# Performance work log

Measured on AMD Instinct MI355X. Metric: run time of the kernel, lower is better.

Reference implementation:

```python
import jax, jax.numpy as jnp
import numpy as np


def setup_inputs() -> dict:
    key = jax.random.key(0)
    k1, k2, k3 = jax.random.split(key, 3)
    B, D, R, O = 8192, 2048, 16, 64
    # small init scale so the 2048-step matrix chain product stays numerically sane
    inputs = jax.random.normal(k1, (B, D), dtype=jnp.float32) * 0.05
    # cores near identity (glorot-scale perturbation) to avoid chain blow-up/collapse
    cores = jnp.eye(R, dtype=jnp.float32)[None] + jax.random.normal(k2, (D, R, R), dtype=jnp.float32) * (1.0 / R)
    projection = jax.random.normal(k3, (R, O), dtype=jnp.float32) * (1.0 / np.sqrt(R))
    bias = jnp.zeros((O,), dtype=jnp.float32)
    return {"inputs": inputs, "cores": cores, "projection": projection, "bias": bias}


def reference(inputs, cores, projection, bias):
    # inputs: (B, D); cores: (D, R, R); projection: (R, O); bias: (O,)
    B = inputs.shape[0]
    R = cores.shape[-1]
    boundary0 = jnp.ones((B, R), dtype=inputs.dtype)  # MPS boundary vector

    x_t = inputs.T  # (D, B) so scan iterates over features

    def step(boundary, xs):
        core, x = xs  # core: (R, R), x: (B,)
        # boundary <- (boundary @ core) scaled by the feature value (A^i[x_i])
        boundary = jnp.matmul(boundary, core) * x[:, None]
        return boundary, None

    boundary, _ = jax.lax.scan(step, boundary0, (cores, x_t))
    out = jnp.matmul(boundary, projection) + bias  # (B, O)
    return out
```

## Files before the change

kernel.cpp:

```cpp
#include <hip/hip_runtime.h>
#include <math.h>


#define DFEAT 2048
#define R 16
#define NR2 256
#define OUTD 64
#define CHUNK 64
#define NCHUNK (DFEAT / CHUNK)
#define MAGIC 0x7E57C0DE

__device__ __forceinline__ float4 rowmul(const float* Arow, const float* B,
                                         int c0) {
    float4 acc = {0.f, 0.f, 0.f, 0.f};
    const float4* a4 = (const float4*)Arow;
#pragma unroll
    for (int kk = 0; kk < 4; ++kk) {
        const float4 av = a4[kk];
        const float4 b0 = *(const float4*)&B[(4 * kk + 0) * 16 + c0];
        const float4 b1 = *(const float4*)&B[(4 * kk + 1) * 16 + c0];
        const float4 b2 = *(const float4*)&B[(4 * kk + 2) * 16 + c0];
        const float4 b3 = *(const float4*)&B[(4 * kk + 3) * 16 + c0];
        acc.x = fmaf(av.x, b0.x, fmaf(av.y, b1.x, fmaf(av.z, b2.x, fmaf(av.w, b3.x, acc.x))));
        acc.y = fmaf(av.x, b0.y, fmaf(av.y, b1.y, fmaf(av.z, b2.y, fmaf(av.w, b3.y, acc.y))));
        acc.z = fmaf(av.x, b0.z, fmaf(av.y, b1.z, fmaf(av.z, b2.z, fmaf(av.w, b3.z, acc.z))));
        acc.w = fmaf(av.x, b0.w, fmaf(av.y, b1.w, fmaf(av.z, b2.w, fmaf(av.w, b3.w, acc.w))));
    }
    return acc;
}

__global__ __launch_bounds__(256) void mps_fused(const float* __restrict__ cores,
                                                 const float* __restrict__ proj,
                                                 const float* __restrict__ x,
                                                 float* __restrict__ prodbuf,
                                                 float* __restrict__ partials,
                                                 int* __restrict__ flags,
                                                 float* __restrict__ pE,
                                                 int B) {
    __shared__ __align__(16) float S[4608];
    float* Bbase = S;
    float* Abase = S + 2048;
    float* Fbase = S + 4096;
    float* Pt    = S;

    const int tid  = threadIdx.x;
    const int wave = tid >> 6, lane = tid & 63;

    if (blockIdx.x >= NCHUNK) {
        const int row = (blockIdx.x - NCHUNK) * 4 + wave;
        if (row >= B) return;
        const float4* xr = (const float4*)(x + (size_t)row * DFEAT);
        float prod = 1.f;
#pragma unroll
        for (int it = 0; it < DFEAT / (64 * 4); ++it) {
            float4 v = xr[it * 64 + lane];
            prod *= (v.x * v.y) * (v.z * v.w);
        }
#pragma unroll
        for (int off = 32; off > 0; off >>= 1)
            prod *= __shfl_xor(prod, off);
        if (lane == 0) prodbuf[row] = prod;
        return;
    }

    const int ri = lane >> 2;
    const int c0 = (lane & 3) << 2;
    const size_t d0 = (size_t)blockIdx.x * CHUNK;

    const float* gw = cores + (d0 + 16 * wave) * NR2;
    float4 pre[16];
#pragma unroll
    for (int t = 0; t < 16; ++t)
        pre[t] = *(const float4*)&gw[(size_t)t * NR2 + lane * 4];

    float* AwW = Abase + wave * 512;
    float* BbW = Bbase + wave * 512;

    *(float4*)&AwW[0 * 256 + lane * 4] = pre[0];
    int cur = 0;
#pragma unroll
    for (int t = 1; t < 16; ++t) {
        *(float4*)&BbW[(t & 1) * 256 + lane * 4] = pre[t];
        float4 r = rowmul(&AwW[cur * 256 + ri * 16], &BbW[(t & 1) * 256], c0);
        *(float4*)&AwW[(cur ^ 1) * 256 + ri * 16 + c0] = r;
        cur ^= 1;
    }
    __syncthreads();

    if (wave == 0) {
        *(float4*)&Fbase[0 * 256 + ri * 16 + c0] =
            *(const float4*)&Abase[0 * 512 + 1 * 256 + ri * 16 + c0];
        int cc = 0;
        for (int w = 1; w < 4; ++w) {
            float4 r = rowmul(&Fbase[cc * 256 + ri * 16],
                              &Abase[w * 512 + 1 * 256], c0);
            *(float4*)&Fbase[(cc ^ 1) * 256 + ri * 16 + c0] = r;
            cc ^= 1;
        }
    }
    __syncthreads();
    const int i = tid >> 4, j = tid & 15;
    const float v = Fbase[1 * 256 + tid];

    if (blockIdx.x != 0) {
        partials[blockIdx.x * NR2 + tid] = v;
        __syncthreads();
        if (tid == 0)
            __hip_atomic_store(&flags[blockIdx.x], MAGIC,
                               __ATOMIC_RELEASE, __HIP_MEMORY_SCOPE_AGENT);
        return;
    }

    Pt[0 * 256 + j * 16 + i] = v;

    {
        const int f = 1 + (tid % (NCHUNK - 1));
        while (__hip_atomic_load(&flags[f], __ATOMIC_ACQUIRE,
                                 __HIP_MEMORY_SCOPE_AGENT) != MAGIC) { }
    }
    __syncthreads();

    float w = 1.f;
    int E = 0;
    for (int rr = 0; rr < 4; ++rr) {
#pragma unroll
        for (int q = 0; q < 2; ++q) {
            const int idx = q * 256 + tid;
            const int flat = idx * 4;
            const int s = flat >> 8;
            if (rr > 0 || s > 0) {
                float4 p4 =
                    ((const float4*)(partials + (size_t)(8 * rr) * NR2))[idx];
                const int e = flat & 255;
                const int k = e >> 4, j0 = e & 15;
                Pt[s * 256 + (j0 + 0) * 16 + k] = p4.x;
                Pt[s * 256 + (j0 + 1) * 16 + k] = p4.y;
                Pt[s * 256 + (j0 + 2) * 16 + k] = p4.z;
                Pt[s * 256 + (j0 + 3) * 16 + k] = p4.w;
            }
        }
        __syncthreads();
        if (tid < 64) {
            const int jj = tid & 15, q = tid >> 4;
            for (int s = 0; s < 8; ++s) {
                const float4 pr = *(const float4*)&Pt[s * 256 + jj * 16 + 4 * q];
                float sum;
                sum = __shfl(w, 4 * q + 0) * pr.x;
                sum = fmaf(__shfl(w, 4 * q + 1), pr.y, sum);
                sum = fmaf(__shfl(w, 4 * q + 2), pr.z, sum);
                sum = fmaf(__shfl(w, 4 * q + 3), pr.w, sum);
                sum += __shfl_xor(sum, 16);
                sum += __shfl_xor(sum, 32);
                w = sum;
            }
            float m = fabsf(w);
#pragma unroll
            for (int off = 1; off <= 8; off <<= 1)
                m = fmaxf(m, __shfl_xor(m, off));
            if (m > 0.f) {
                int e2 = 0;
                (void)frexpf(m, &e2);
                w = ldexpf(w, -e2);
                E += e2;
            }
        }
        __syncthreads();
    }

    if (tid < 64) {
        float p = 0.f;
#pragma unroll
        for (int k = 0; k < R; ++k)
            p = fmaf(__shfl(w, k), proj[k * OUTD + tid], p);
        pE[tid] = p;
        if (tid == 0) ((int*)pE)[OUTD] = E;
    }
}

__global__ __launch_bounds__(256) void mps_scale(const float* __restrict__ prodbuf,
                                                 const float* __restrict__ pE,
                                                 const float* __restrict__ bias,
                                                 float* __restrict__ out,
                                                 int B) {
    const int idx = blockIdx.x * 256 + threadIdx.x;
    const int total4 = B * (OUTD / 4);
    if (idx >= total4) return;
    const int row = idx >> 4;
    const int c4  = idx & 15;
    const float pr = prodbuf[row];
    const int   E  = ((const int*)pE)[OUTD];
    const float4 pe = ((const float4*)pE)[c4];
    const float4 bb = ((const float4*)bias)[c4];
    float4 r;
    r.x = ldexpf(pe.x * pr, E) + bb.x;
    r.y = ldexpf(pe.y * pr, E) + bb.y;
    r.z = ldexpf(pe.z * pr, E) + bb.z;
    r.w = ldexpf(pe.w * pr, E) + bb.w;
    ((float4*)out)[idx] = r;
}

extern "C" void kernel_launch(void* const* d_in, const int* in_sizes, int n_in,
                              void* d_out, int out_size, void* d_ws, size_t ws_size,
                              hipStream_t stream) {
    const float* inputs = (const float*)d_in[0];
    const float* cores  = (const float*)d_in[1];
    const float* proj   = (const float*)d_in[2];
    const float* bias   = (const float*)d_in[3];
    float* out = (float*)d_out;

    const int B = in_sizes[0] / DFEAT;

    float* prodbuf  = (float*)d_ws;
    float* partials = prodbuf + B;
    float* pE    = partials + NCHUNK * NR2;
    int*   flags = (int*)(pE + 68);

    const int rowBlocks = (B + 3) / 4;
    mps_fused<<<NCHUNK + rowBlocks, 256, 0, stream>>>(cores, proj, inputs,
                                                      prodbuf, partials, flags,
                                                      pE, B);
    mps_scale<<<(B * 16 + 255) / 256, 256, 0, stream>>>(prodbuf, pE, bias,
                                                        out, B);
}
```

Measured before the change: 103.7 us.

## Fuse output scaling into main kernel using per-unit readiness flags

Merges the separate scaling kernel into the main kernel: row-product blocks publish per-unit flags, and each of the 32 chain blocks waits for its rows and for the final projected vector, then writes its slice of the output. This removes a kernel launch and the inter-kernel gap. In exchange, output writing is confined to 32 blocks, and spin-waits and stale-flag reliance across calls add risk.

```diff
diff --git a/kernel.cpp b/kernel.cpp
--- a/kernel.cpp
+++ b/kernel.cpp
@@ -29,14 +29,17 @@
     return acc;
 }
 
-__global__ __launch_bounds__(256) void mps_fused(const float* __restrict__ cores,
-                                                 const float* __restrict__ proj,
-                                                 const float* __restrict__ x,
-                                                 float* __restrict__ prodbuf,
-                                                 float* __restrict__ partials,
-                                                 int* __restrict__ flags,
-                                                 float* __restrict__ pE,
-                                                 int B) {
+__global__ __launch_bounds__(256, 8) void mps_one(const float* __restrict__ cores,
+                                                  const float* __restrict__ proj,
+                                                  const float* __restrict__ x,
+                                                  const float* __restrict__ bias,
+                                                  float* __restrict__ out,
+                                                  float* __restrict__ prodbuf,
+                                                  float* __restrict__ partials,
+                                                  int* __restrict__ flags,
+                                                  int* __restrict__ uflags,
+                                                  float* __restrict__ pE,
+                                                  int B) {
     __shared__ __align__(16) float S[4608];
     float* Bbase = S;
     float* Abase = S + 2048;
@@ -45,10 +48,13 @@
 
     const int tid  = threadIdx.x;
     const int wave = tid >> 6, lane = tid & 63;
-
-    if (blockIdx.x >= NCHUNK) {
-        const int row = (blockIdx.x - NCHUNK) * 4 + wave;
-        if (row >= B) return;
+    const int bid  = blockIdx.x;
+    const int nunits = B >> 2;
+    const int UPC = nunits / NCHUNK;
+
+    if (bid >= NCHUNK) {
+        const int u = bid - NCHUNK;
+        const int row = u * 4 + wave;
         const float4* xr = (const float4*)(x + (size_t)row * DFEAT);
         float prod = 1.f;
 #pragma unroll
@@ -60,12 +66,16 @@
         for (int off = 32; off > 0; off >>= 1)
             prod *= __shfl_xor(prod, off);
         if (lane == 0) prodbuf[row] = prod;
+        __syncthreads();
+        if (tid == 0)
+            __hip_atomic_store(&uflags[u], MAGIC,
+                               __ATOMIC_RELEASE, __HIP_MEMORY_SCOPE_AGENT);
         return;
     }
 
     const int ri = lane >> 2;
     const int c0 = (lane & 3) << 2;
-    const size_t d0 = (size_t)blockIdx.x * CHUNK;
+    const size_t d0 = (size_t)bid * CHUNK;
 
     const float* gw = cores + (d0 + 16 * wave) * NR2;
     float4 pre[16];
@@ -102,101 +112,122 @@
     const int i = tid >> 4, j = tid & 15;
     const float v = Fbase[1 * 256 + tid];
 
-    if (blockIdx.x != 0) {
-        partials[blockIdx.x * NR2 + tid] = v;
+    if (bid != 0) {
+        partials[bid * NR2 + tid] = v;
         __syncthreads();
         if (tid == 0)
-            __hip_atomic_store(&flags[blockIdx.x], MAGIC,
+            __hip_atomic_store(&flags[bid], MAGIC,
                                __ATOMIC_RELEASE, __HIP_MEMORY_SCOPE_AGENT);
-        return;
-    }
-
-    Pt[0 * 256 + j * 16 + i] = v;
-
-    {
-        const int f = 1 + (tid % (NCHUNK - 1));
-        while (__hip_atomic_load(&flags[f], __ATOMIC_ACQUIRE,
-                                 __HIP_MEMORY_SCOPE_AGENT) != MAGIC) { }
-    }
-    __syncthreads();
-
-    float w = 1.f;
-    int E = 0;
-    for (int rr = 0; rr < 4; ++rr) {
-#pragma unroll
-        for (int q = 0; q < 2; ++q) {
-            const int idx = q * 256 + tid;
-            const int flat = idx * 4;
-            const int s = flat >> 8;
-            if (rr > 0 || s > 0) {
-                float4 p4 =
-                    ((const float4*)(partials + (size_t)(8 * rr) * NR2))[idx];
-                const int e = flat & 255;
-                const int k = e >> 4, j0 = e & 15;
-                Pt[s * 256 + (j0 + 0) * 16 + k] = p4.x;
-                Pt[s * 256 + (j0 + 1) * 16 + k] = p4.y;
-                Pt[s * 256 + (j0 + 2) * 16 + k] = p4.z;
-                Pt[s * 256 + (j0 + 3) * 16 + k] = p4.w;
+    } else {
+        Pt[0 * 256 + j * 16 + i] = v;
+
+        {
+            const int f = 1 + (tid % (NCHUNK - 1));
+            while (__hip_atomic_load(&flags[f], __ATOMIC_ACQUIRE,
+                                     __HIP_MEMORY_SCOPE_AGENT) != MAGIC) { }
+        }
+        __syncthreads();
+
+        float w = 1.f;
+        int E = 0;
+        for (int rr = 0; rr < 4; ++rr) {
+#pragma unroll
+            for (int q = 0; q < 2; ++q) {
+                const int idx = q * 256 + tid;
+                const int flat = idx * 4;
+                const int s = flat >> 8;
+                if (rr > 0 || s > 0) {
+                    float4 p4 = ((const float4*)(partials +
+                                   (size_t)(8 * rr) * NR2))[idx];
+                    const int e = flat & 255;
+                    const int k = e >> 4, j0 = e & 15;
+                    Pt[s * 256 + (j0 + 0) * 16 + k] = p4.x;
+                    Pt[s * 256 + (j0 + 1) * 16 + k] = p4.y;
+                    Pt[s * 256 + (j0 + 2) * 16 + k] = p4.z;
+                    Pt[s * 256 + (j0 + 3) * 16 + k] = p4.w;
+                }
             }
-        }
-        __syncthreads();
+            __syncthreads();
+            if (tid < 64) {
+                const int jj = tid & 15, q = tid >> 4;
+                for (int s = 0; s < 8; ++s) {
+                    const float4 pr =
+                        *(const float4*)&Pt[s * 256 + jj * 16 + 4 * q];
+                    float sum;
+                    sum = __shfl(w, 4 * q + 0) * pr.x;
+                    sum = fmaf(__shfl(w, 4 * q + 1), pr.y, sum);
+                    sum = fmaf(__shfl(w, 4 * q + 2), pr.z, sum);
+                    sum = fmaf(__shfl(w, 4 * q + 3), pr.w, sum);
+                    sum += __shfl_xor(sum, 16);
+                    sum += __shfl_xor(sum, 32);
+                    w = sum;
+                }
+                float m = fabsf(w);
+#pragma unroll
+                for (int off = 1; off <= 8; off <<= 1)
+                    m = fmaxf(m, __shfl_xor(m, off));
+                if (m > 0.f) {
+                    int e2 = 0;
+                    (void)frexpf(m, &e2);
+                    w = ldexpf(w, -e2);
+                    E += e2;
+                }
+            }
+            __syncthreads();
+        }
+
         if (tid < 64) {
-            const int jj = tid & 15, q = tid >> 4;
-            for (int s = 0; s < 8; ++s) {
-                const float4 pr = *(const float4*)&Pt[s * 256 + jj * 16 + 4 * q];
-                float sum;
-                sum = __shfl(w, 4 * q + 0) * pr.x;
-                sum = fmaf(__shfl(w, 4 * q + 1), pr.y, sum);
-                sum = fmaf(__shfl(w, 4 * q + 2), pr.z, sum);
-                sum = fmaf(__shfl(w, 4 * q + 3), pr.w, sum);
-                sum += __shfl_xor(sum, 16);
-                sum += __shfl_xor(sum, 32);
-                w = sum;
-            }
-            float m = fabsf(w);
-#pragma unroll
-            for (int off = 1; off <= 8; off <<= 1)
-                m = fmaxf(m, __shfl_xor(m, off));
-            if (m > 0.f) {
-                int e2 = 0;
-                (void)frexpf(m, &e2);
-                w = ldexpf(w, -e2);
-                E += e2;
-            }
-        }
-        __syncthreads();
+            float p = 0.f;
+#pragma unroll
+            for (int k = 0; k < R; ++k)
+                p = fmaf(__shfl(w, k), proj[k * OUTD + tid], p);
+            pE[tid] = p;
+            if (tid == 0) ((int*)pE)[OUTD] = E;
+        }
+        __syncthreads();
+        if (tid == 0)
+            __hip_atomic_store(&flags[0], MAGIC,
+                               __ATOMIC_RELEASE, __HIP_MEMORY_SCOPE_AGENT);
     }
 
     if (tid < 64) {
-        float p = 0.f;
-#pragma unroll
-        for (int k = 0; k < R; ++k)
-            p = fmaf(__shfl(w, k), proj[k * OUTD + tid], p);
-        pE[tid] = p;
-        if (tid == 0) ((int*)pE)[OUTD] = E;
-    }
-}
-
-__global__ __launch_bounds__(256) void mps_scale(const float* __restrict__ prodbuf,
-                                                 const float* __restrict__ pE,
-                                                 const float* __restrict__ bias,
-                                                 float* __restrict__ out,
-                                                 int B) {
-    const int idx = blockIdx.x * 256 + threadIdx.x;
-    const int total4 = B * (OUTD / 4);
-    if (idx >= total4) return;
-    const int row = idx >> 4;
-    const int c4  = idx & 15;
-    const float pr = prodbuf[row];
-    const int   E  = ((const int*)pE)[OUTD];
-    const float4 pe = ((const float4*)pE)[c4];
-    const float4 bb = ((const float4*)bias)[c4];
-    float4 r;
-    r.x = ldexpf(pe.x * pr, E) + bb.x;
-    r.y = ldexpf(pe.y * pr, E) + bb.y;
-    r.z = ldexpf(pe.z * pr, E) + bb.z;
-    r.w = ldexpf(pe.w * pr, E) + bb.w;
-    ((float4*)out)[idx] = r;
+        for (int i2 = tid; i2 < UPC; i2 += 64) {
+            while (__hip_atomic_load(&uflags[bid * UPC + i2], __ATOMIC_ACQUIRE,
+                                     __HIP_MEMORY_SCOPE_AGENT) != MAGIC)
+                __builtin_amdgcn_s_sleep(16);
+        }
+    } else if (tid == 64) {
+        while (__hip_atomic_load(&flags[0], __ATOMIC_ACQUIRE,
+                                 __HIP_MEMORY_SCOPE_AGENT) != MAGIC)
+            __builtin_amdgcn_s_sleep(16);
+    }
+    __syncthreads();
+    (void)__hip_atomic_load(&flags[0], __ATOMIC_ACQUIRE,
+                            __HIP_MEMORY_SCOPE_AGENT);
+
+    if (tid < 16) {
+        ((float4*)&Fbase[0])[tid]  = ((const float4*)pE)[tid];
+        ((float4*)&Fbase[64])[tid] = ((const float4*)bias)[tid];
+    }
+    if (tid == 16) ((int*)&Fbase[128])[0] = ((const int*)pE)[OUTD];
+    __syncthreads();
+    const int   E  = ((const int*)&Fbase[128])[0];
+    const float4 pe = ((const float4*)&Fbase[0])[tid & 15];
+    const float4 bb = ((const float4*)&Fbase[64])[tid & 15];
+
+    const int chunk4 = B * (OUTD / 4) / NCHUNK;
+    const int base4  = bid * chunk4;
+    float4* o4 = (float4*)out;
+    for (int q = 0; q < chunk4 / 256; ++q) {
+        const int idx = base4 + q * 256 + tid;
+        const float pr = prodbuf[idx >> 4];
+        float4 r;
+        r.x = ldexpf(pe.x * pr, E) + bb.x;
+        r.y = ldexpf(pe.y * pr, E) + bb.y;
+        r.z = ldexpf(pe.z * pr, E) + bb.z;
+        r.w = ldexpf(pe.w * pr, E) + bb.w;
+        o4[idx] = r;
+    }
 }
 
 extern "C" void kernel_launch(void* const* d_in, const int* in_sizes, int n_in,
@@ -214,11 +245,10 @@
     float* partials = prodbuf + B;
     float* pE    = partials + NCHUNK * NR2;
     int*   flags = (int*)(pE + 68);
-
-    const int rowBlocks = (B + 3) / 4;
-    mps_fused<<<NCHUNK + rowBlocks, 256, 0, stream>>>(cores, proj, inputs,
-                                                      prodbuf, partials, flags,
-                                                      pE, B);
-    mps_scale<<<(B * 16 + 255) / 256, 256, 0, stream>>>(prodbuf, pE, bias,
-                                                        out, B);
+    int*   uflags = flags + NCHUNK;
+
+    const int nunits = B / 4;
+    mps_one<<<NCHUNK + nunits, 256, 0, stream>>>(cores, proj, inputs, bias,
+                                                 out, prodbuf, partials,
+                                                 flags, uflags, pE, B);
 }
```

Result: slower. 164.5 us (+58.6%).

## Split chain kernel from row products and fuse row product with output scaling

Applied to the files above, without the earlier changes.

The row-product blocks move out of the chain-reduction kernel into a new per-row kernel. That kernel computes each row's product of x and writes the scaled, biased output directly. This removes the prodbuf intermediate and its write/read round trip. The trade-off is that the bandwidth-heavy read of x no longer overlaps with the latency-bound chain reduction; it now runs serially after it.

```diff
diff --git a/kernel.cpp b/kernel.cpp
--- a/kernel.cpp
+++ b/kernel.cpp
@@ -29,14 +29,11 @@
     return acc;
 }
 
-__global__ __launch_bounds__(256) void mps_fused(const float* __restrict__ cores,
+__global__ __launch_bounds__(256) void mps_chain(const float* __restrict__ cores,
                                                  const float* __restrict__ proj,
-                                                 const float* __restrict__ x,
-                                                 float* __restrict__ prodbuf,
                                                  float* __restrict__ partials,
                                                  int* __restrict__ flags,
-                                                 float* __restrict__ pE,
-                                                 int B) {
+                                                 float* __restrict__ pE) {
     __shared__ __align__(16) float S[4608];
     float* Bbase = S;
     float* Abase = S + 2048;
@@ -45,24 +42,6 @@
 
     const int tid  = threadIdx.x;
     const int wave = tid >> 6, lane = tid & 63;
-
-    if (blockIdx.x >= NCHUNK) {
-        const int row = (blockIdx.x - NCHUNK) * 4 + wave;
-        if (row >= B) return;
-        const float4* xr = (const float4*)(x + (size_t)row * DFEAT);
-        float prod = 1.f;
-#pragma unroll
-        for (int it = 0; it < DFEAT / (64 * 4); ++it) {
-            float4 v = xr[it * 64 + lane];
-            prod *= (v.x * v.y) * (v.z * v.w);
-        }
-#pragma unroll
-        for (int off = 32; off > 0; off >>= 1)
-            prod *= __shfl_xor(prod, off);
-        if (lane == 0) prodbuf[row] = prod;
-        return;
-    }
-
     const int ri = lane >> 2;
     const int c0 = (lane & 3) << 2;
     const size_t d0 = (size_t)blockIdx.x * CHUNK;
@@ -177,26 +156,30 @@
     }
 }
 
-__global__ __launch_bounds__(256) void mps_scale(const float* __restrict__ prodbuf,
-                                                 const float* __restrict__ pE,
-                                                 const float* __restrict__ bias,
-                                                 float* __restrict__ out,
-                                                 int B) {
-    const int idx = blockIdx.x * 256 + threadIdx.x;
-    const int total4 = B * (OUTD / 4);
-    if (idx >= total4) return;
-    const int row = idx >> 4;
-    const int c4  = idx & 15;
-    const float pr = prodbuf[row];
+__global__ __launch_bounds__(256) void mps_rows(const float* __restrict__ x,
+                                                const float* __restrict__ pE,
+                                                const float* __restrict__ bias,
+                                                float* __restrict__ out,
+                                                int B) {
+    const int gtid = blockIdx.x * 256 + threadIdx.x;
+    const int row  = gtid >> 6;
+    const int lane = threadIdx.x & 63;
+    if (row >= B) return;
+
+    const float4* xr = (const float4*)(x + (size_t)row * DFEAT);
+    float prod = 1.f;
+#pragma unroll
+    for (int it = 0; it < DFEAT / (64 * 4); ++it) {
+        float4 v = xr[it * 64 + lane];
+        prod *= (v.x * v.y) * (v.z * v.w);
+    }
+#pragma unroll
+    for (int off = 32; off > 0; off >>= 1)
+        prod *= __shfl_xor(prod, off);
+
+    const float pv = pE[lane];
     const int   E  = ((const int*)pE)[OUTD];
-    const float4 pe = ((const float4*)pE)[c4];
-    const float4 bb = ((const float4*)bias)[c4];
-    float4 r;
-    r.x = ldexpf(pe.x * pr, E) + bb.x;
-    r.y = ldexpf(pe.y * pr, E) + bb.y;
-    r.z = ldexpf(pe.z * pr, E) + bb.z;
-    r.w = ldexpf(pe.w * pr, E) + bb.w;
-    ((float4*)out)[idx] = r;
+    out[(size_t)row * OUTD + lane] = ldexpf(pv * prod, E) + bias[lane];
 }
 
 extern "C" void kernel_launch(void* const* d_in, const int* in_sizes, int n_in,
@@ -210,15 +193,11 @@
 
     const int B = in_sizes[0] / DFEAT;
 
-    float* prodbuf  = (float*)d_ws;
-    float* partials = prodbuf + B;
+    float* partials = (float*)d_ws;
     float* pE    = partials + NCHUNK * NR2;
     int*   flags = (int*)(pE + 68);
 
-    const int rowBlocks = (B + 3) / 4;
-    mps_fused<<<NCHUNK + rowBlocks, 256, 0, stream>>>(cores, proj, inputs,
-                                                      prodbuf, partials, flags,
-                                                      pE, B);
-    mps_scale<<<(B * 16 + 255) / 256, 256, 0, stream>>>(prodbuf, pE, bias,
-                                                        out, B);
-}
+    mps_chain<<<NCHUNK, 256, 0, stream>>>(cores, proj, partials, flags, pE);
+    mps_rows<<<(B * 64 + 255) / 256, 256, 0, stream>>>(inputs, pE, bias,
+                                                       out, B);
+}
```

New measurement: 107.4 us. +3.6%, slower.
